# Performance work log

Hardware: AMD Instinct MI355X
Metric: run time of the kernel (lower is better)

## Reference

```python
import jax, jax.numpy as jnp
import numpy as np
import math

D_MODEL = 1024
NHEAD = 16
D_K = D_MODEL // NHEAD
B, S = 4, 2048


def _stable_softmax(scores):
    # faithful to the source: max-subtract, exp, divide by (sum + 1e-10)
    m = jnp.max(scores, axis=-1, keepdims=True)
    e = jnp.exp(scores - m)
    return e / (jnp.sum(e, axis=-1, keepdims=True) + 1e-10)


def setup_inputs() -> dict:
    key = jax.random.key(0)
    ks = jax.random.split(key, 11)
    gain = math.sqrt(2.0)
    # xavier_uniform: bound = gain * sqrt(6/(fan_in+fan_out)) = gain*sqrt(6/(2*d))
    bound = gain * math.sqrt(6.0 / (2 * D_MODEL))
    def xavier(k):
        return jax.random.uniform(k, (D_MODEL, D_MODEL), jnp.float32, -bound, bound)
    return {
        "q": jax.random.normal(ks[0], (B, S, D_MODEL), jnp.float32),
        "k": jax.random.normal(ks[1], (B, S, D_MODEL), jnp.float32),
        "v": jax.random.normal(ks[2], (B, S, D_MODEL), jnp.float32),
        "Wq": xavier(ks[3]), "bq": jnp.zeros((D_MODEL,), jnp.float32),
        "Wk": xavier(ks[4]), "bk": jnp.zeros((D_MODEL,), jnp.float32),
        "Wv": xavier(ks[5]), "bv": jnp.zeros((D_MODEL,), jnp.float32),
        "Wo": xavier(ks[6]), "bo": jnp.zeros((D_MODEL,), jnp.float32),
    }


def reference(q, k, v, Wq, bq, Wk, bk, Wv, bv, Wo, bo):
    b = q.shape[0]
    # linear projections (torch Linear: x @ W.T + b)
    Q = q @ Wq.T + bq
    K = k @ Wk.T + bk
    V = v @ Wv.T + bv
    # [B, H, S, d_k]
    Q = Q.reshape(b, -1, NHEAD, D_K).transpose(0, 2, 1, 3)
    K = K.reshape(b, -1, NHEAD, D_K).transpose(0, 2, 1, 3)
    V = V.reshape(b, -1, NHEAD, D_K).transpose(0, 2, 1, 3)
    scores = jnp.einsum("bhqd,bhkd->bhqk", Q / math.sqrt(D_K), K)
    attn_weight = _stable_softmax(scores)  # dropout p=0 -> identity
    attn = jnp.einsum("bhqk,bhkd->bhqd", attn_weight, V)
    concat = attn.transpose(0, 2, 1, 3).reshape(b, -1, D_MODEL)
    return concat @ Wo.T + bo
```

## Files before the change

kernel.cpp:

```cpp
#include <hip/hip_runtime.h>

#define DMODEL 1024
#define NH 16
#define DK 64
#define NB 4
#define SEQ 2048
#define MTOT (NB*SEQ)

typedef __attribute__((ext_vector_type(8))) short bf16x8;
typedef __attribute__((ext_vector_type(4))) float f32x4;
typedef __attribute__((ext_vector_type(4))) float f4;
typedef __attribute__((ext_vector_type(4))) unsigned short us4;
typedef __attribute__((ext_vector_type(8))) unsigned short us8;
typedef const __attribute__((address_space(1))) void* as1cv;
typedef __attribute__((address_space(3))) void* as3v;

__device__ __forceinline__ unsigned short f2bf(float f){
  union { float f; unsigned u; } v; v.f = f;
  unsigned r = v.u + 0x7FFFu + ((v.u >> 16) & 1u);
  return (unsigned short)(r >> 16);
}

__global__ __launch_bounds__(256) void cvt_kernel(const float* __restrict__ src,
                                                  unsigned short* __restrict__ dst, int n4){
  int i = blockIdx.x*256 + threadIdx.x;
  if (i >= n4) return;
  f4 f = ((const f4*)src)[i];
  us4 o;
  o.x = f2bf(f.x); o.y = f2bf(f.y); o.z = f2bf(f.z); o.w = f2bf(f.w);
  ((us4*)dst)[i] = o;
}

template<int MODE, int AF32>
__global__ __launch_bounds__(256) void gemm_bt(const void* __restrict__ Aptr,
    const unsigned short* __restrict__ Bw, const float* __restrict__ bias,
    void* __restrict__ dst, float scale)
{
  __shared__ __align__(16) unsigned short sA[128*32];
  __shared__ __align__(16) unsigned short sB[128*32];
  const int tid = threadIdx.x;
  const int lane = tid & 63;
  const int w = tid >> 6;
  const int m0 = blockIdx.y * 128;
  const int n0 = blockIdx.x * 128;
  const int fr = lane & 15;
  const int kg = lane >> 4;
  const int msub = (w & 1) * 64;
  const int nsub = (w >> 1) * 64;

  f32x4 acc[4][4];
#pragma unroll
  for (int i = 0; i < 4; i++)
#pragma unroll
    for (int j = 0; j < 4; j++) acc[i][j] = f32x4{0.f,0.f,0.f,0.f};

  for (int kt = 0; kt < DMODEL; kt += 32){
#pragma unroll
    for (int j = 0; j < 2; j++){
      const int idx = j*256 + tid;
      const int row = idx >> 2;
      const int cg  = (idx & 3) << 3;
      if (AF32){
        const float* ap = (const float*)Aptr + (size_t)(m0+row)*DMODEL + kt + cg;
        f4 f0 = *(const f4*)ap;
        f4 f1 = *(const f4*)(ap + 4);
        us8 o;
        o[0]=f2bf(f0.x); o[1]=f2bf(f0.y); o[2]=f2bf(f0.z); o[3]=f2bf(f0.w);
        o[4]=f2bf(f1.x); o[5]=f2bf(f1.y); o[6]=f2bf(f1.z); o[7]=f2bf(f1.w);
        *((us8*)sA + idx) = o;
      } else {
        const unsigned short* ap = (const unsigned short*)Aptr + (size_t)(m0+row)*DMODEL + kt + cg;
        __builtin_amdgcn_global_load_lds((as1cv)ap, (as3v)(&sA[(size_t)idx*8]), 16, 0, 0);
      }
      const unsigned short* bp = Bw + (size_t)(n0+row)*DMODEL + kt + cg;
      __builtin_amdgcn_global_load_lds((as1cv)bp, (as3v)(&sB[(size_t)idx*8]), 16, 0, 0);
    }
    __syncthreads();
    bf16x8 af[4], bfr[4];
#pragma unroll
    for (int f = 0; f < 4; f++)
      af[f] = *(const bf16x8*)&sA[(msub + f*16 + fr)*32 + kg*8];
#pragma unroll
    for (int f = 0; f < 4; f++)
      bfr[f] = *(const bf16x8*)&sB[(nsub + f*16 + fr)*32 + kg*8];
#pragma unroll
    for (int i = 0; i < 4; i++)
#pragma unroll
      for (int j = 0; j < 4; j++)
        acc[i][j] = __builtin_amdgcn_mfma_f32_16x16x32_bf16(af[i], bfr[j], acc[i][j], 0, 0, 0);
    __syncthreads();
  }

#pragma unroll
  for (int i = 0; i < 4; i++){
#pragma unroll
    for (int j = 0; j < 4; j++){
      const int n = n0 + nsub + j*16 + fr;
      const float bv = bias[n];
#pragma unroll
      for (int r = 0; r < 4; r++){
        const int m = m0 + msub + i*16 + kg*4 + r;
        float vacc = acc[i][j][r] + bv;
        if (MODE == 2){
          ((float*)dst)[(size_t)m*DMODEL + n] = vacc;
        } else {
          const int b = m >> 11, s = m & (SEQ-1);
          const int h = n >> 6,  d = n & (DK-1);
          ((unsigned short*)dst)[((size_t)(b*NH + h)*SEQ + s)*DK + d] = f2bf(vacc * scale);
        }
      }
    }
  }
}

__global__ __launch_bounds__(256) void attn_kernel(const unsigned short* __restrict__ Qh,
    const unsigned short* __restrict__ Kh, const unsigned short* __restrict__ Vh,
    unsigned short* __restrict__ attnO)
{
  __shared__ __align__(16) unsigned short sVT[64*72];
  __shared__ __align__(16) unsigned short sP[4*16*64];
  const int tid = threadIdx.x;
  const int lane = tid & 63;
  const int w = tid >> 6;
  const int fr = lane & 15;
  const int kg = lane >> 4;
  const int bh = blockIdx.y;
  const int qt = blockIdx.x*64 + w*16;

  const unsigned short* Qb = Qh + ((size_t)bh*SEQ + qt)*DK;
  const unsigned short* Kb = Kh + (size_t)bh*SEQ*DK;
  const unsigned short* Vb = Vh + (size_t)bh*SEQ*DK;

  bf16x8 qf0 = *(const bf16x8*)(Qb + fr*DK + kg*8);
  bf16x8 qf1 = *(const bf16x8*)(Qb + fr*DK + 32 + kg*8);

  f32x4 o[4];
  float mr[4], lr[4];
#pragma unroll
  for (int n = 0; n < 4; n++) o[n] = f32x4{0.f,0.f,0.f,0.f};
#pragma unroll
  for (int r = 0; r < 4; r++){ mr[r] = -1e30f; lr[r] = 0.f; }

  unsigned short* Pw = sP + w*(16*64);
  const int vk = tid & 63;
  const int vg = tid >> 6;

  for (int kt = 0; kt < SEQ; kt += 64){
    __syncthreads();
#pragma unroll
    for (int half = 0; half < 2; half++){
      const int dg = half*4 + vg;
      us8 vv = *(const us8*)(Vb + (size_t)(kt + vk)*DK + dg*8);
#pragma unroll
      for (int i2 = 0; i2 < 8; i2++)
        sVT[(dg*8 + i2)*72 + vk] = vv[i2];
    }
    __syncthreads();

    f32x4 s[4];
#pragma unroll
    for (int n = 0; n < 4; n++){
      const unsigned short* kp = Kb + (size_t)(kt + n*16 + fr)*DK + kg*8;
      bf16x8 k0 = *(const bf16x8*)kp;
      bf16x8 k1 = *(const bf16x8*)(kp + 32);
      f32x4 z = f32x4{0.f,0.f,0.f,0.f};
      z    = __builtin_amdgcn_mfma_f32_16x16x32_bf16(qf0, k0, z, 0, 0, 0);
      s[n] = __builtin_amdgcn_mfma_f32_16x16x32_bf16(qf1, k1, z, 0, 0, 0);
    }

    float tm[4];
#pragma unroll
    for (int r = 0; r < 4; r++)
      tm[r] = fmaxf(fmaxf(s[0][r], s[1][r]), fmaxf(s[2][r], s[3][r]));
#pragma unroll
    for (int msk = 1; msk < 16; msk <<= 1){
#pragma unroll
      for (int r = 0; r < 4; r++) tm[r] = fmaxf(tm[r], __shfl_xor(tm[r], msk));
    }
    float al[4], rs[4];
#pragma unroll
    for (int r = 0; r < 4; r++){
      float mn = fmaxf(mr[r], tm[r]);
      al[r] = __expf(mr[r] - mn);
      mr[r] = mn;
      rs[r] = 0.f;
    }
#pragma unroll
    for (int n = 0; n < 4; n++){
#pragma unroll
      for (int r = 0; r < 4; r++){
        float p = __expf(s[n][r] - mr[r]);
        rs[r] += p;
        const int row  = kg*4 + r;
        const int colb = (n*32 + fr*2) ^ ((row & 7) << 4);
        *(unsigned short*)((char*)Pw + row*128 + colb) = f2bf(p);
      }
    }
#pragma unroll
    for (int msk = 1; msk < 16; msk <<= 1){
#pragma unroll
      for (int r = 0; r < 4; r++) rs[r] += __shfl_xor(rs[r], msk);
    }
    f32x4 alv;
#pragma unroll
    for (int r = 0; r < 4; r++){ lr[r] = lr[r]*al[r] + rs[r]; alv[r] = al[r]; }
#pragma unroll
    for (int n = 0; n < 4; n++) o[n] *= alv;

    bf16x8 pf0 = *(const bf16x8*)((char*)Pw + fr*128 + (( 0 + kg*16) ^ ((fr & 7) << 4)));
    bf16x8 pf1 = *(const bf16x8*)((char*)Pw + fr*128 + ((64 + kg*16) ^ ((fr & 7) << 4)));
#pragma unroll
    for (int n = 0; n < 4; n++){
      const unsigned short* vtp = &sVT[(n*16 + fr)*72 + kg*8];
      bf16x8 v0 = *(const bf16x8*)vtp;
      bf16x8 v1 = *(const bf16x8*)(vtp + 32);
      o[n] = __builtin_amdgcn_mfma_f32_16x16x32_bf16(pf0, v0, o[n], 0, 0, 0);
      o[n] = __builtin_amdgcn_mfma_f32_16x16x32_bf16(pf1, v1, o[n], 0, 0, 0);
    }
  }

  const int b = bh >> 4, h = bh & (NH-1);
#pragma unroll
  for (int r = 0; r < 4; r++){
    const float inv = 1.f / (lr[r] + 1e-10f);
    const int srow = qt + kg*4 + r;
    const size_t base = ((size_t)b*SEQ + srow)*DMODEL + (size_t)h*DK;
#pragma unroll
    for (int n = 0; n < 4; n++)
      attnO[base + n*16 + fr] = f2bf(o[n][r] * inv);
  }
}

extern "C" void kernel_launch(void* const* d_in, const int* in_sizes, int n_in,
                              void* d_out, int out_size, void* d_ws, size_t ws_size,
                              hipStream_t stream)
{
  const float* q  = (const float*)d_in[0];
  const float* k  = (const float*)d_in[1];
  const float* v  = (const float*)d_in[2];
  const float* Wq = (const float*)d_in[3];
  const float* bq = (const float*)d_in[4];
  const float* Wk = (const float*)d_in[5];
  const float* bk = (const float*)d_in[6];
  const float* Wv = (const float*)d_in[7];
  const float* bv = (const float*)d_in[8];
  const float* Wo = (const float*)d_in[9];
  const float* bo = (const float*)d_in[10];

  char* ws = (char*)d_ws;
  const size_t WSZ = (size_t)DMODEL*DMODEL*2;
  const size_t SZ  = (size_t)MTOT*DMODEL*2;
  unsigned short* wqb   = (unsigned short*)(ws);
  unsigned short* wkb   = (unsigned short*)(ws + WSZ);
  unsigned short* wvb   = (unsigned short*)(ws + 2*WSZ);
  unsigned short* wob   = (unsigned short*)(ws + 3*WSZ);
  unsigned short* Qh    = (unsigned short*)(ws + 4*WSZ);
  unsigned short* Kh    = (unsigned short*)(ws + 4*WSZ + SZ);
  unsigned short* Vh    = (unsigned short*)(ws + 4*WSZ + 2*SZ);
  unsigned short* attnB = (unsigned short*)(ws + 4*WSZ + 3*SZ);

  const int n4 = DMODEL*DMODEL/4;
  cvt_kernel<<<n4/256, 256, 0, stream>>>(Wq, wqb, n4);
  cvt_kernel<<<n4/256, 256, 0, stream>>>(Wk, wkb, n4);
  cvt_kernel<<<n4/256, 256, 0, stream>>>(Wv, wvb, n4);
  cvt_kernel<<<n4/256, 256, 0, stream>>>(Wo, wob, n4);

  dim3 gproj(DMODEL/128, MTOT/128);
  gemm_bt<0,1><<<gproj, 256, 0, stream>>>(q, wqb, bq, Qh, 0.125f);
  gemm_bt<0,1><<<gproj, 256, 0, stream>>>(k, wkb, bk, Kh, 1.0f);
  gemm_bt<0,1><<<gproj, 256, 0, stream>>>(v, wvb, bv, Vh, 1.0f);

  attn_kernel<<<dim3(SEQ/64, NB*NH), 256, 0, stream>>>(Qh, Kh, Vh, attnB);

  gemm_bt<2,0><<<gproj, 256, 0, stream>>>(attnB, wob, bo, d_out, 1.0f);
}
```

Before: 494.9 us.

## Rewrite attention: V pre-transposed by projection, S^T MFMA, register P, lazy rescale

The V projection now writes V transposed per head, so the attention kernel reads V^T fragments straight from global memory. This removes the shared-memory transpose and its two barriers. Attention computes S^T = K·Q^T so that P stays in registers and feeds 16x16x16 MFMAs directly, with no shared-memory round trip. Each wave handles 32 query rows, the grid is swizzled, softmax uses exp2 with log2e folded into the Q scale, and rescaling is skipped when the max grows by at most 8. The trade-offs are uncoalesced 8-byte V loads straight from global memory and more registers per thread.

```diff
diff --git a/kernel.cpp b/kernel.cpp
--- a/kernel.cpp
+++ b/kernel.cpp
@@ -8,10 +8,12 @@
 #define MTOT (NB*SEQ)
 
 typedef __attribute__((ext_vector_type(8))) short bf16x8;
+typedef __attribute__((ext_vector_type(4))) short s16x4;
 typedef __attribute__((ext_vector_type(4))) float f32x4;
 typedef __attribute__((ext_vector_type(4))) float f4;
 typedef __attribute__((ext_vector_type(4))) unsigned short us4;
 typedef __attribute__((ext_vector_type(8))) unsigned short us8;
+typedef __attribute__((ext_vector_type(2))) unsigned int u32x2;
 typedef const __attribute__((address_space(1))) void* as1cv;
 typedef __attribute__((address_space(3))) void* as3v;
 
@@ -19,6 +21,21 @@
   union { float f; unsigned u; } v; v.f = f;
   unsigned r = v.u + 0x7FFFu + ((v.u >> 16) & 1u);
   return (unsigned short)(r >> 16);
+}
+
+__device__ __forceinline__ unsigned cvt_pk_bf16(float lo, float hi){
+  unsigned r;
+  asm("v_cvt_pk_bf16_f32 %0, %1, %2" : "=v"(r) : "v"(lo), "v"(hi));
+  return r;
+}
+
+__device__ __forceinline__ f32x4 mfma16(s16x4 a, s16x4 b, f32x4 c){
+#if __has_builtin(__builtin_amdgcn_mfma_f32_16x16x16bf16_1k)
+  return __builtin_amdgcn_mfma_f32_16x16x16bf16_1k(a, b, c, 0, 0, 0);
+#else
+  asm("v_mfma_f32_16x16x16_bf16 %0, %1, %2, %0" : "+v"(c) : "v"(a), "v"(b));
+  return c;
+#endif
 }
 
 __global__ __launch_bounds__(256) void cvt_kernel(const float* __restrict__ src,
@@ -97,16 +114,26 @@
     for (int j = 0; j < 4; j++){
       const int n = n0 + nsub + j*16 + fr;
       const float bv = bias[n];
-#pragma unroll
-      for (int r = 0; r < 4; r++){
-        const int m = m0 + msub + i*16 + kg*4 + r;
-        float vacc = acc[i][j][r] + bv;
-        if (MODE == 2){
-          ((float*)dst)[(size_t)m*DMODEL + n] = vacc;
-        } else {
-          const int b = m >> 11, s = m & (SEQ-1);
-          const int h = n >> 6,  d = n & (DK-1);
-          ((unsigned short*)dst)[((size_t)(b*NH + h)*SEQ + s)*DK + d] = f2bf(vacc * scale);
+      if (MODE == 1){
+        const int m = m0 + msub + i*16 + kg*4;
+        const int b = m >> 11, s = m & (SEQ-1);
+        const int h = n >> 6,  d = n & (DK-1);
+        us4 pk;
+#pragma unroll
+        for (int r = 0; r < 4; r++) pk[r] = f2bf(acc[i][j][r] + bv);
+        *(us4*)&((unsigned short*)dst)[((size_t)(b*NH+h)*DK + d)*SEQ + s] = pk;
+      } else {
+#pragma unroll
+        for (int r = 0; r < 4; r++){
+          const int m = m0 + msub + i*16 + kg*4 + r;
+          float vacc = acc[i][j][r] + bv;
+          if (MODE == 2){
+            ((float*)dst)[(size_t)m*DMODEL + n] = vacc;
+          } else {
+            const int b = m >> 11, s = m & (SEQ-1);
+            const int h = n >> 6,  d = n & (DK-1);
+            ((unsigned short*)dst)[((size_t)(b*NH + h)*SEQ + s)*DK + d] = f2bf(vacc * scale);
+          }
         }
       }
     }
@@ -114,120 +141,129 @@
 }
 
 __global__ __launch_bounds__(256) void attn_kernel(const unsigned short* __restrict__ Qh,
-    const unsigned short* __restrict__ Kh, const unsigned short* __restrict__ Vh,
+    const unsigned short* __restrict__ Kh, const unsigned short* __restrict__ VTh,
     unsigned short* __restrict__ attnO)
 {
-  __shared__ __align__(16) unsigned short sVT[64*72];
-  __shared__ __align__(16) unsigned short sP[4*16*64];
   const int tid = threadIdx.x;
   const int lane = tid & 63;
   const int w = tid >> 6;
   const int fr = lane & 15;
   const int kg = lane >> 4;
-  const int bh = blockIdx.y;
-  const int qt = blockIdx.x*64 + w*16;
+  const int bid = blockIdx.x;
+  const int swz = (bid & 7) * 128 + (bid >> 3);
+  const int bh = swz >> 4;
+  const int qt = (swz & 15) * 128 + w * 32;
 
   const unsigned short* Qb = Qh + ((size_t)bh*SEQ + qt)*DK;
-  const unsigned short* Kb = Kh + (size_t)bh*SEQ*DK;
-  const unsigned short* Vb = Vh + (size_t)bh*SEQ*DK;
-
-  bf16x8 qf0 = *(const bf16x8*)(Qb + fr*DK + kg*8);
-  bf16x8 qf1 = *(const bf16x8*)(Qb + fr*DK + 32 + kg*8);
-
-  f32x4 o[4];
-  float mr[4], lr[4];
-#pragma unroll
-  for (int n = 0; n < 4; n++) o[n] = f32x4{0.f,0.f,0.f,0.f};
-#pragma unroll
-  for (int r = 0; r < 4; r++){ mr[r] = -1e30f; lr[r] = 0.f; }
-
-  unsigned short* Pw = sP + w*(16*64);
-  const int vk = tid & 63;
-  const int vg = tid >> 6;
+  const unsigned short* Kb = Kh + (size_t)bh*SEQ*DK + (size_t)fr*DK + kg*8;
+  const unsigned short* Vb = VTh + (size_t)bh*DK*SEQ + kg*4;
+
+  bf16x8 qf[2][2];
+#pragma unroll
+  for (int qh = 0; qh < 2; qh++){
+    qf[qh][0] = *(const bf16x8*)(Qb + (qh*16 + fr)*DK + kg*8);
+    qf[qh][1] = *(const bf16x8*)(Qb + (qh*16 + fr)*DK + 32 + kg*8);
+  }
+
+  f32x4 o[2][4];
+#pragma unroll
+  for (int qh = 0; qh < 2; qh++)
+#pragma unroll
+    for (int nd = 0; nd < 4; nd++) o[qh][nd] = f32x4{0.f,0.f,0.f,0.f};
+  float mr[2] = {-1e30f, -1e30f};
+  float lr[2] = {0.f, 0.f};
 
   for (int kt = 0; kt < SEQ; kt += 64){
-    __syncthreads();
-#pragma unroll
-    for (int half = 0; half < 2; half++){
-      const int dg = half*4 + vg;
-      us8 vv = *(const us8*)(Vb + (size_t)(kt + vk)*DK + dg*8);
-#pragma unroll
-      for (int i2 = 0; i2 < 8; i2++)
-        sVT[(dg*8 + i2)*72 + vk] = vv[i2];
-    }
-    __syncthreads();
-
-    f32x4 s[4];
+    f32x4 s[2][4];
 #pragma unroll
     for (int n = 0; n < 4; n++){
-      const unsigned short* kp = Kb + (size_t)(kt + n*16 + fr)*DK + kg*8;
+      const unsigned short* kp = Kb + (size_t)(kt + n*16)*DK;
       bf16x8 k0 = *(const bf16x8*)kp;
       bf16x8 k1 = *(const bf16x8*)(kp + 32);
-      f32x4 z = f32x4{0.f,0.f,0.f,0.f};
-      z    = __builtin_amdgcn_mfma_f32_16x16x32_bf16(qf0, k0, z, 0, 0, 0);
-      s[n] = __builtin_amdgcn_mfma_f32_16x16x32_bf16(qf1, k1, z, 0, 0, 0);
-    }
-
-    float tm[4];
-#pragma unroll
-    for (int r = 0; r < 4; r++)
-      tm[r] = fmaxf(fmaxf(s[0][r], s[1][r]), fmaxf(s[2][r], s[3][r]));
-#pragma unroll
-    for (int msk = 1; msk < 16; msk <<= 1){
-#pragma unroll
-      for (int r = 0; r < 4; r++) tm[r] = fmaxf(tm[r], __shfl_xor(tm[r], msk));
-    }
-    float al[4], rs[4];
+#pragma unroll
+      for (int qh = 0; qh < 2; qh++){
+        f32x4 z = f32x4{0.f,0.f,0.f,0.f};
+        z         = __builtin_amdgcn_mfma_f32_16x16x32_bf16(k0, qf[qh][0], z, 0, 0, 0);
+        s[qh][n]  = __builtin_amdgcn_mfma_f32_16x16x32_bf16(k1, qf[qh][1], s[qh][n] = z, 0, 0, 0);
+      }
+    }
+
+    unsigned pk[2][4][2];
+#pragma unroll
+    for (int qh = 0; qh < 2; qh++){
+      float tm = -1e30f;
+#pragma unroll
+      for (int n = 0; n < 4; n++)
+#pragma unroll
+        for (int r = 0; r < 4; r++) tm = fmaxf(tm, s[qh][n][r]);
+      tm = fmaxf(tm, __shfl_xor(tm, 16));
+      tm = fmaxf(tm, __shfl_xor(tm, 32));
+      const bool defer = __all(tm - mr[qh] <= 8.0f);
+      float aal = 1.0f;
+      if (!defer){
+        const float mn = fmaxf(mr[qh], tm);
+        aal = exp2f(mr[qh] - mn);
+        mr[qh] = mn;
+      }
+      float p[4][4];
+      float rs = 0.f;
+#pragma unroll
+      for (int n = 0; n < 4; n++)
+#pragma unroll
+        for (int r = 0; r < 4; r++){
+          p[n][r] = exp2f(s[qh][n][r] - mr[qh]);
+          rs += p[n][r];
+        }
+      rs += __shfl_xor(rs, 16);
+      rs += __shfl_xor(rs, 32);
+      lr[qh] = lr[qh]*aal + rs;
+      if (!defer){
+        f32x4 alv;
+#pragma unroll
+        for (int r = 0; r < 4; r++) alv[r] = __shfl(aal, kg*4 + r, 64);
+#pragma unroll
+        for (int nd = 0; nd < 4; nd++) o[qh][nd] *= alv;
+      }
+#pragma unroll
+      for (int n = 0; n < 4; n++){
+        pk[qh][n][0] = cvt_pk_bf16(p[n][0], p[n][1]);
+        pk[qh][n][1] = cvt_pk_bf16(p[n][2], p[n][3]);
+      }
+    }
+
+#pragma unroll
+    for (int nd = 0; nd < 4; nd++){
+      const unsigned short* vp = Vb + (size_t)(nd*16 + fr)*SEQ + kt;
+      s16x4 vf[4];
+#pragma unroll
+      for (int ks = 0; ks < 4; ks++) vf[ks] = *(const s16x4*)(vp + ks*16);
+#pragma unroll
+      for (int ks = 0; ks < 4; ks++){
+#pragma unroll
+        for (int qh = 0; qh < 2; qh++){
+          union { u32x2 u; s16x4 s; } pa;
+          pa.u = u32x2{pk[qh][ks][0], pk[qh][ks][1]};
+          o[qh][nd] = mfma16(pa.s, vf[ks], o[qh][nd]);
+        }
+      }
+    }
+  }
+
+  const int b = bh >> 4, h = bh & (NH-1);
+#pragma unroll
+  for (int qh = 0; qh < 2; qh++){
+    const float invl = 1.f / (lr[qh] + 1e-10f);
+    f32x4 iv;
+#pragma unroll
+    for (int r = 0; r < 4; r++) iv[r] = __shfl(invl, kg*4 + r, 64);
 #pragma unroll
     for (int r = 0; r < 4; r++){
-      float mn = fmaxf(mr[r], tm[r]);
-      al[r] = __expf(mr[r] - mn);
-      mr[r] = mn;
-      rs[r] = 0.f;
-    }
-#pragma unroll
-    for (int n = 0; n < 4; n++){
-#pragma unroll
-      for (int r = 0; r < 4; r++){
-        float p = __expf(s[n][r] - mr[r]);
-        rs[r] += p;
-        const int row  = kg*4 + r;
-        const int colb = (n*32 + fr*2) ^ ((row & 7) << 4);
-        *(unsigned short*)((char*)Pw + row*128 + colb) = f2bf(p);
-      }
-    }
-#pragma unroll
-    for (int msk = 1; msk < 16; msk <<= 1){
-#pragma unroll
-      for (int r = 0; r < 4; r++) rs[r] += __shfl_xor(rs[r], msk);
-    }
-    f32x4 alv;
-#pragma unroll
-    for (int r = 0; r < 4; r++){ lr[r] = lr[r]*al[r] + rs[r]; alv[r] = al[r]; }
-#pragma unroll
-    for (int n = 0; n < 4; n++) o[n] *= alv;
-
-    bf16x8 pf0 = *(const bf16x8*)((char*)Pw + fr*128 + (( 0 + kg*16) ^ ((fr & 7) << 4)));
-    bf16x8 pf1 = *(const bf16x8*)((char*)Pw + fr*128 + ((64 + kg*16) ^ ((fr & 7) << 4)));
-#pragma unroll
-    for (int n = 0; n < 4; n++){
-      const unsigned short* vtp = &sVT[(n*16 + fr)*72 + kg*8];
-      bf16x8 v0 = *(const bf16x8*)vtp;
-      bf16x8 v1 = *(const bf16x8*)(vtp + 32);
-      o[n] = __builtin_amdgcn_mfma_f32_16x16x32_bf16(pf0, v0, o[n], 0, 0, 0);
-      o[n] = __builtin_amdgcn_mfma_f32_16x16x32_bf16(pf1, v1, o[n], 0, 0, 0);
-    }
-  }
-
-  const int b = bh >> 4, h = bh & (NH-1);
-#pragma unroll
-  for (int r = 0; r < 4; r++){
-    const float inv = 1.f / (lr[r] + 1e-10f);
-    const int srow = qt + kg*4 + r;
-    const size_t base = ((size_t)b*SEQ + srow)*DMODEL + (size_t)h*DK;
-#pragma unroll
-    for (int n = 0; n < 4; n++)
-      attnO[base + n*16 + fr] = f2bf(o[n][r] * inv);
+      const int srow = qt + qh*16 + kg*4 + r;
+      const size_t base = ((size_t)b*SEQ + srow)*DMODEL + (size_t)h*DK;
+#pragma unroll
+      for (int nd = 0; nd < 4; nd++)
+        attnO[base + nd*16 + fr] = f2bf(o[qh][nd][r] * iv[r]);
+    }
   }
 }
 
@@ -256,7 +292,7 @@
   unsigned short* wob   = (unsigned short*)(ws + 3*WSZ);
   unsigned short* Qh    = (unsigned short*)(ws + 4*WSZ);
   unsigned short* Kh    = (unsigned short*)(ws + 4*WSZ + SZ);
-  unsigned short* Vh    = (unsigned short*)(ws + 4*WSZ + 2*SZ);
+  unsigned short* VTh   = (unsigned short*)(ws + 4*WSZ + 2*SZ);
   unsigned short* attnB = (unsigned short*)(ws + 4*WSZ + 3*SZ);
 
   const int n4 = DMODEL*DMODEL/4;
@@ -266,11 +302,11 @@
   cvt_kernel<<<n4/256, 256, 0, stream>>>(Wo, wob, n4);
 
   dim3 gproj(DMODEL/128, MTOT/128);
-  gemm_bt<0,1><<<gproj, 256, 0, stream>>>(q, wqb, bq, Qh, 0.125f);
+  gemm_bt<0,1><<<gproj, 256, 0, stream>>>(q, wqb, bq, Qh, 0.125f*1.44269504088896f);
   gemm_bt<0,1><<<gproj, 256, 0, stream>>>(k, wkb, bk, Kh, 1.0f);
-  gemm_bt<0,1><<<gproj, 256, 0, stream>>>(v, wvb, bv, Vh, 1.0f);
-
-  attn_kernel<<<dim3(SEQ/64, NB*NH), 256, 0, stream>>>(Qh, Kh, Vh, attnB);
+  gemm_bt<1,1><<<gproj, 256, 0, stream>>>(v, wvb, bv, VTh, 1.0f);
+
+  attn_kernel<<<1024, 256, 0, stream>>>(Qh, Kh, VTh, attnB);
 
   gemm_bt<2,0><<<gproj, 256, 0, stream>>>(attnB, wob, bo, d_out, 1.0f);
 }
```

Result: slower. 539.0 us (+8.9%).
